# Performance work log

Hardware: AMD Instinct MI355X
Metric: run time of the kernel (lower is better)

Reference implementation:

```python
import jax, jax.numpy as jnp
import numpy as np

N_HEADS = 16


def setup_inputs() -> dict:
    key = jax.random.key(0)
    k1, k2, k3 = jax.random.split(key, 3)
    B, T, C = 4, 2048, 1024
    x = jax.random.normal(k1, (B, T, C), dtype=jnp.float32)
    # nn.Linear weights: init ~ U(-1/sqrt(fan_in), 1/sqrt(fan_in)); scaled normal is fine for a reference
    w_qkv = jax.random.normal(k2, (C, 3 * C), dtype=jnp.float32) * (1.0 / np.sqrt(C))
    w_out = jax.random.normal(k3, (C, C), dtype=jnp.float32) * (1.0 / np.sqrt(C))
    return {"x": x, "w_qkv": w_qkv, "w_out": w_out}


def reference(x, w_qkv, w_out):
    B, T, C = x.shape
    H = N_HEADS
    D = C // H  # head_dim
    qkv = x @ w_qkv  # [B, T, 3C]
    q, k, v = jnp.split(qkv, 3, axis=-1)
    # [B, H, T, D]
    q = q.reshape(B, T, H, D).transpose(0, 2, 1, 3)
    k = k.reshape(B, T, H, D).transpose(0, 2, 1, 3)
    v = v.reshape(B, T, H, D).transpose(0, 2, 1, 3)
    scale = 1.0 / np.sqrt(D)
    scores = jnp.einsum('bhqd,bhkd->bhqk', q, k) * scale  # [B, H, T, T]
    causal = jnp.tril(jnp.ones((T, T), dtype=bool))
    scores = jnp.where(causal[None, None, :, :], scores, -jnp.inf)
    weights = jax.nn.softmax(scores, axis=-1)
    out = jnp.einsum('bhqk,bhkd->bhqd', weights, v)  # [B, H, T, D]
    out = out.transpose(0, 2, 1, 3).reshape(B, T, C)
    return out @ w_out
```

## Files before the change

kernel.cpp:

```cpp
#include <hip/hip_runtime.h>
#include <hip/hip_bf16.h>
#include <math.h>
#include <type_traits>

using s16x8 = __attribute__((ext_vector_type(8))) short;
using s16x4 = __attribute__((ext_vector_type(4))) short;
using f32x4 = __attribute__((ext_vector_type(4))) float;
using f32x16 = __attribute__((ext_vector_type(16))) float;
using u32 = unsigned int;
using u32x4 = __attribute__((ext_vector_type(4))) u32;

static __device__ __forceinline__ short f2bf(float f) {
  union { float f; unsigned u; } v; v.f = f;
  unsigned r = v.u + 0x7fff + ((v.u >> 16) & 1);
  return (short)(r >> 16);
}

static __device__ __forceinline__ unsigned cvt_pk_bf16(float lo, float hi) {
  unsigned r;
  asm("v_cvt_pk_bf16_f32 %0, %1, %2" : "=v"(r) : "v"(lo), "v"(hi));
  return r;
}

#define GLOAD_LDS(gsrc, ldst)                                                      \
  __builtin_amdgcn_global_load_lds(                                                \
      (const __attribute__((address_space(1))) void*)(gsrc),                       \
      (__attribute__((address_space(3))) void*)(ldst), 16, 0, 0)

__global__ void cast_f32_bf16(const float* __restrict__ in, short* __restrict__ out, int n4) {
  int i = blockIdx.x * blockDim.x + threadIdx.x;
  int stride = gridDim.x * blockDim.x;
  for (int idx = i; idx < n4; idx += stride) {
    float4 v = reinterpret_cast<const float4*>(in)[idx];
    s16x4 o; o[0] = f2bf(v.x); o[1] = f2bf(v.y); o[2] = f2bf(v.z); o[3] = f2bf(v.w);
    reinterpret_cast<s16x4*>(out)[idx] = o;
  }
}

__global__ void transpose_cast(const float* __restrict__ in, short* __restrict__ out, int R, int C) {
  __shared__ float tile[32][33];
  int cb = blockIdx.x * 32, rb = blockIdx.y * 32;
  int tx = threadIdx.x, ty = threadIdx.y;
  #pragma unroll
  for (int i = 0; i < 32; i += 8)
    tile[ty + i][tx] = in[(size_t)(rb + ty + i) * C + cb + tx];
  __syncthreads();
  #pragma unroll
  for (int i = 0; i < 32; i += 8)
    out[(size_t)(cb + ty + i) * R + rb + tx] = f2bf(tile[tx][ty + i]);
}

template <typename OutT, bool VFUSE>
__global__ __launch_bounds__(256) void gemm_bt(const short* __restrict__ A,
                                               const short* __restrict__ BT,
                                               OutT* __restrict__ C,
                                               short* __restrict__ vtOut,
                                               int M, int N, int K, int ldc) {
  __shared__ __align__(16) short As[128][32];
  __shared__ __align__(16) short Bs[128][32];
  const int t = threadIdx.x;
  const int lane = t & 63, wid = t >> 6;
  const int wm = wid >> 1, wn = wid & 1;
  const int bm = blockIdx.y * 128, bn = blockIdx.x * 128;
  const int lr = lane & 15, lg = lane >> 4;

  f32x4 acc[4][4] = {};

  for (int k0 = 0; k0 < K; k0 += 32) {
    #pragma unroll
    for (int rnd = 0; rnd < 2; ++rnd) {
      int chunk = rnd * 256 + t;
      int row = chunk >> 2, c8 = (chunk & 3) * 8;
      GLOAD_LDS(&A[(size_t)(bm + row) * K + k0 + c8], &As[rnd * 64 + wid * 16][0]);
      GLOAD_LDS(&BT[(size_t)(bn + row) * K + k0 + c8], &Bs[rnd * 64 + wid * 16][0]);
    }
    __syncthreads();
    s16x8 af[4], bfr[4];
    #pragma unroll
    for (int i = 0; i < 4; ++i)
      af[i] = *reinterpret_cast<s16x8*>(&As[wm * 64 + i * 16 + lr][lg * 8]);
    #pragma unroll
    for (int j = 0; j < 4; ++j)
      bfr[j] = *reinterpret_cast<s16x8*>(&Bs[wn * 64 + j * 16 + lr][lg * 8]);
    #pragma unroll
    for (int i = 0; i < 4; ++i)
      #pragma unroll
      for (int j = 0; j < 4; ++j)
        acc[i][j] = __builtin_amdgcn_mfma_f32_16x16x32_bf16(af[i], bfr[j], acc[i][j], 0, 0, 0);
    __syncthreads();
  }

  const int r0 = bm + wm * 64, c0 = bn + wn * 64;
  if (!VFUSE || c0 < 2048) {
    #pragma unroll
    for (int i = 0; i < 4; ++i)
      #pragma unroll
      for (int j = 0; j < 4; ++j)
        #pragma unroll
        for (int r = 0; r < 4; ++r) {
          int row = r0 + i * 16 + lg * 4 + r;
          int col = c0 + j * 16 + lr;
          float v = acc[i][j][r];
          if constexpr (std::is_same<OutT, short>::value)
            C[(size_t)row * ldc + col] = f2bf(v);
          else
            C[(size_t)row * ldc + col] = v;
        }
  } else {
    const int bb = bm >> 11;
    #pragma unroll
    for (int i = 0; i < 4; ++i) {
      int tok = (bm & 2047) + wm * 64 + i * 16 + lg * 4;
      #pragma unroll
      for (int j = 0; j < 4; ++j) {
        int col = c0 + j * 16 + lr;
        s16x4 p;
        #pragma unroll
        for (int r = 0; r < 4; ++r) p[r] = f2bf(acc[i][j][r]);
        *reinterpret_cast<s16x4*>(vtOut + (size_t)(bb * 1024 + col - 2048) * 2048 + tok) = p;
      }
    }
  }
}

__global__ __launch_bounds__(256, 3) void attn_kernel(const short* __restrict__ qk,
                                                      const short* __restrict__ vt,
                                                      short* __restrict__ att) {
  const int T = 2048, C2 = 2048, Cc = 1024;
  const int fid = blockIdx.x;
  const int qb = 15 - (fid >> 6);
  const int bh = fid & 63;
  const int h = bh & 15, b = bh >> 4;
  const int t = threadIdx.x;
  const int w = t >> 6, l = t & 63;
  const int q2 = l & 31, hi = l >> 5;

  __shared__ __align__(16) short Ks[2][64 * 64];
  __shared__ __align__(16) short Vts[2][64 * 64];

  const int qrow_base = qb * 128 + w * 32;
  const int qrow = qrow_base + q2;
  const int tmax = 2 * qb + (w >> 1);
  const int nt = 2 * qb + 2;

  const float SC = 0.125f * 1.44269504088896340736f;
  s16x8 aq[4];
  #pragma unroll
  for (int ds = 0; ds < 4; ++ds) {
    s16x8 q = *reinterpret_cast<const s16x8*>(
        qk + (size_t)(b * T + qrow) * C2 + h * 64 + ds * 16 + hi * 8);
    #pragma unroll
    for (int j = 0; j < 8; ++j) {
      union { float f; unsigned u; } v; v.u = ((unsigned)(unsigned short)q[j]) << 16;
      q[j] = f2bf(v.f * SC);
    }
    aq[ds] = q;
  }

  f32x16 o[2] = {};
  float mst = -INFINITY, lst = 0.f;

  const int srow = w * 16 + (l >> 3);
  const int srcc8 = ((l & 7) ^ (l >> 3)) * 8;
  const short* kp = qk + (size_t)(b * T + srow) * C2 + Cc + h * 64 + srcc8;
  const short* vp = vt + (size_t)(bh * 64 + srow) * T + srcc8;

  auto stage = [&](int buf) {
    GLOAD_LDS(kp,           &Ks[buf][(w * 16) * 64]);
    GLOAD_LDS(kp + 8 * C2,  &Ks[buf][(w * 16 + 8) * 64]);
    GLOAD_LDS(vp,           &Vts[buf][(w * 16) * 64]);
    GLOAD_LDS(vp + 8 * T,   &Vts[buf][(w * 16 + 8) * 64]);
    kp += 64 * C2;
    vp += 64;
  };

  stage(0);
  for (int tt = 0; tt < nt; ++tt) {
    __syncthreads();
    if (tt + 1 < nt) stage((tt + 1) & 1);
    if (tt > tmax) continue;
    const int j0 = tt << 6;
    const short* K_ = &Ks[tt & 1][0];
    const short* V_ = &Vts[tt & 1][0];

    f32x16 st[2];
    __builtin_amdgcn_s_setprio(1);
    #pragma unroll
    for (int kt = 0; kt < 2; ++kt) {
      f32x16 s = {};
      #pragma unroll
      for (int ds = 0; ds < 4; ++ds) {
        int row = kt * 32 + q2;
        s16x8 ak = *reinterpret_cast<const s16x8*>(
            &K_[row * 64 + (((ds * 2 + hi) ^ (row & 7)) * 8)]);
        s = __builtin_amdgcn_mfma_f32_32x32x16_bf16(ak, aq[ds], s, 0, 0, 0);
      }
      st[kt] = s;
    }
    __builtin_amdgcn_s_setprio(0);

    if (j0 + 63 > qrow_base) {
      #pragma unroll
      for (int kt = 0; kt < 2; ++kt)
        #pragma unroll
        for (int r = 0; r < 16; ++r) {
          int key = j0 + kt * 32 + (r & 3) + 8 * (r >> 2) + 4 * hi;
          if (key > qrow) st[kt][r] = -INFINITY;
        }
    }

    float a16[16];
    #pragma unroll
    for (int r = 0; r < 16; ++r) a16[r] = fmaxf(st[0][r], st[1][r]);
    #pragma unroll
    for (int r = 0; r < 8; ++r) a16[r] = fmaxf(a16[r], a16[r + 8]);
    #pragma unroll
    for (int r = 0; r < 4; ++r) a16[r] = fmaxf(a16[r], a16[r + 4]);
    float mx = fmaxf(fmaxf(a16[0], a16[1]), fmaxf(a16[2], a16[3]));
    mx = fmaxf(mx, __shfl_xor(mx, 32));
    const bool resc = !__all(mx - mst <= 8.f);
    if (resc) {
      float mn = fmaxf(mst, mx);
      float corr = exp2f(mst - mn);
      mst = mn;
      lst *= corr;
      #pragma unroll
      for (int dt = 0; dt < 2; ++dt)
        #pragma unroll
        for (int r = 0; r < 16; ++r) o[dt][r] *= corr;
    }
    #pragma unroll
    for (int kt = 0; kt < 2; ++kt)
      #pragma unroll
      for (int r = 0; r < 16; ++r) st[kt][r] = exp2f(st[kt][r] - mst);
    float sv[16];
    #pragma unroll
    for (int r = 0; r < 16; ++r) sv[r] = st[0][r] + st[1][r];
    #pragma unroll
    for (int r = 0; r < 8; ++r) sv[r] += sv[r + 8];
    #pragma unroll
    for (int r = 0; r < 4; ++r) sv[r] += sv[r + 4];
    float ps = (sv[0] + sv[1]) + (sv[2] + sv[3]);
    ps += __shfl_xor(ps, 32);
    lst += ps;

    s16x8 pb[4];
    #pragma unroll
    for (int kt = 0; kt < 2; ++kt)
      #pragma unroll
      for (int s = 0; s < 2; ++s) {
        unsigned w01 = cvt_pk_bf16(st[kt][s * 8 + 0], st[kt][s * 8 + 1]);
        unsigned w23 = cvt_pk_bf16(st[kt][s * 8 + 2], st[kt][s * 8 + 3]);
        unsigned w45 = cvt_pk_bf16(st[kt][s * 8 + 4], st[kt][s * 8 + 5]);
        unsigned w67 = cvt_pk_bf16(st[kt][s * 8 + 6], st[kt][s * 8 + 7]);
        asm("v_permlane32_swap_b32 %0, %1" : "+v"(w01), "+v"(w45));
        asm("v_permlane32_swap_b32 %0, %1" : "+v"(w23), "+v"(w67));
        u32x4 f; f[0] = w01; f[1] = w23; f[2] = w45; f[3] = w67;
        pb[kt * 2 + s] = *reinterpret_cast<s16x8*>(&f);
      }

    __builtin_amdgcn_s_setprio(1);
    #pragma unroll
    for (int dt = 0; dt < 2; ++dt) {
      int row = dt * 32 + q2;
      #pragma unroll
      for (int ks = 0; ks < 4; ++ks) {
        s16x8 av = *reinterpret_cast<const s16x8*>(
            &V_[row * 64 + (((ks * 2 + hi) ^ (row & 7)) * 8)]);
        o[dt] = __builtin_amdgcn_mfma_f32_32x32x16_bf16(av, pb[ks], o[dt], 0, 0, 0);
      }
    }
    __builtin_amdgcn_s_setprio(0);
  }

  __syncthreads();
  u32* osm = reinterpret_cast<u32*>(&Ks[0][0]) + w * 1024;
  float inv = 1.f / lst;
  #pragma unroll
  for (int dt = 0; dt < 2; ++dt)
    #pragma unroll
    for (int p = 0; p < 8; ++p) {
      unsigned pk = ((unsigned)(unsigned short)f2bf(o[dt][2 * p + 1] * inv) << 16)
                  | (unsigned)(unsigned short)f2bf(o[dt][2 * p] * inv);
      int col = dt * 16 + (p >> 1) * 4 + 2 * hi + (p & 1);
      int chunk = col >> 2, inc = col & 3;
      osm[q2 * 32 + ((chunk ^ (q2 & 7)) * 4) + inc] = pk;
    }
  #pragma unroll
  for (int c = 0; c < 4; ++c) {
    int chunk = hi * 4 + c;
    u32x4 v4 = *reinterpret_cast<u32x4*>(&osm[q2 * 32 + ((chunk ^ (q2 & 7)) * 4)]);
    *reinterpret_cast<u32x4*>(
        att + (size_t)(b * T + qrow_base + q2) * Cc + h * 64 + chunk * 8) = v4;
  }
}

extern "C" void kernel_launch(void* const* d_in, const int* in_sizes, int n_in,
                              void* d_out, int out_size, void* d_ws, size_t ws_size,
                              hipStream_t stream) {
  const float* x     = (const float*)d_in[0];
  const float* w_qkv = (const float*)d_in[1];
  const float* w_out = (const float*)d_in[2];
  float* out = (float*)d_out;

  char* ws = (char*)d_ws;
  short* xb    = (short*)(ws);
  short* wqkvT = (short*)(ws + 16777216);
  short* woT   = (short*)(ws + 23068672);
  short* qk    = (short*)(ws + 25165824);
  short* vtb   = (short*)(ws + 58720256);
  short* att   = (short*)(ws + 75497472);

  cast_f32_bf16<<<2048, 256, 0, stream>>>(x, xb, (8192 * 1024) / 4);
  transpose_cast<<<dim3(3072 / 32, 1024 / 32), dim3(32, 8), 0, stream>>>(w_qkv, wqkvT, 1024, 3072);
  transpose_cast<<<dim3(1024 / 32, 1024 / 32), dim3(32, 8), 0, stream>>>(w_out, woT, 1024, 1024);

  gemm_bt<short, true><<<dim3(3072 / 128, 8192 / 128), 256, 0, stream>>>(
      xb, wqkvT, qk, vtb, 8192, 3072, 1024, 2048);
  attn_kernel<<<1024, 256, 0, stream>>>(qk, vtb, att);
  gemm_bt<float, false><<<dim3(1024 / 128, 8192 / 128), 256, 0, stream>>>(
      att, woT, out, nullptr, 8192, 1024, 1024, 1024);
}
```

Before: 194.9 us.

## Double-buffer GEMM LDS tiles with BK=64, XOR swizzle, and block remap

Restructures the bf16 GEMM main loop to use two LDS buffers with a K-tile of 64, so the global-to-LDS load of the next tile overlaps the MFMA work on the current one and one barrier per iteration is removed. LDS rows are XOR-swizzled by row index to avoid bank conflicts on the fragment reads. Workgroup IDs are remapped in groups of 8, which is meant to improve L2 locality or spread tiles across XCDs. LDS usage grows fourfold, which may reduce occupancy.

```diff
diff --git a/kernel.cpp b/kernel.cpp
--- a/kernel.cpp
+++ b/kernel.cpp
@@ -56,38 +56,62 @@
                                                OutT* __restrict__ C,
                                                short* __restrict__ vtOut,
                                                int M, int N, int K, int ldc) {
-  __shared__ __align__(16) short As[128][32];
-  __shared__ __align__(16) short Bs[128][32];
+  __shared__ __align__(16) short As[2][128 * 64];
+  __shared__ __align__(16) short Bs[2][128 * 64];
   const int t = threadIdx.x;
   const int lane = t & 63, wid = t >> 6;
   const int wm = wid >> 1, wn = wid & 1;
-  const int bm = blockIdx.y * 128, bn = blockIdx.x * 128;
   const int lr = lane & 15, lg = lane >> 4;
 
+  const int gx = gridDim.x;
+  const int nwg = gx * gridDim.y;
+  int fid = blockIdx.y * gx + blockIdx.x;
+  fid = (fid & 7) * (nwg >> 3) + (fid >> 3);
+  const int bn = (fid % gx) * 128;
+  const int bm = (fid / gx) * 128;
+
+  const int srow = lane >> 3;
+  const int schunk = (lane & 7) ^ srow;
+  const short* ap = A + (size_t)(bm + wid * 8 + srow) * K + schunk * 8;
+  const short* bp = BT + (size_t)(bn + wid * 8 + srow) * K + schunk * 8;
+
   f32x4 acc[4][4] = {};
-
-  for (int k0 = 0; k0 < K; k0 += 32) {
-    #pragma unroll
-    for (int rnd = 0; rnd < 2; ++rnd) {
-      int chunk = rnd * 256 + t;
-      int row = chunk >> 2, c8 = (chunk & 3) * 8;
-      GLOAD_LDS(&A[(size_t)(bm + row) * K + k0 + c8], &As[rnd * 64 + wid * 16][0]);
-      GLOAD_LDS(&BT[(size_t)(bn + row) * K + k0 + c8], &Bs[rnd * 64 + wid * 16][0]);
-    }
+  const int nk = K >> 6;
+
+  auto stage = [&](int buf, int kt) {
+    const size_t ko = (size_t)kt << 6;
+    #pragma unroll
+    for (int j = 0; j < 4; ++j) {
+      GLOAD_LDS(ap + (size_t)j * 32 * K + ko, &As[buf][(j * 32 + wid * 8) * 64]);
+      GLOAD_LDS(bp + (size_t)j * 32 * K + ko, &Bs[buf][(j * 32 + wid * 8) * 64]);
+    }
+  };
+
+  stage(0, 0);
+  for (int kt = 0; kt < nk; ++kt) {
     __syncthreads();
-    s16x8 af[4], bfr[4];
-    #pragma unroll
-    for (int i = 0; i < 4; ++i)
-      af[i] = *reinterpret_cast<s16x8*>(&As[wm * 64 + i * 16 + lr][lg * 8]);
-    #pragma unroll
-    for (int j = 0; j < 4; ++j)
-      bfr[j] = *reinterpret_cast<s16x8*>(&Bs[wn * 64 + j * 16 + lr][lg * 8]);
-    #pragma unroll
-    for (int i = 0; i < 4; ++i)
-      #pragma unroll
-      for (int j = 0; j < 4; ++j)
-        acc[i][j] = __builtin_amdgcn_mfma_f32_16x16x32_bf16(af[i], bfr[j], acc[i][j], 0, 0, 0);
-    __syncthreads();
+    if (kt + 1 < nk) stage((kt + 1) & 1, kt + 1);
+    const short* A_ = &As[kt & 1][0];
+    const short* B_ = &Bs[kt & 1][0];
+    #pragma unroll
+    for (int ks = 0; ks < 2; ++ks) {
+      s16x8 af[4], bfr[4];
+      #pragma unroll
+      for (int i = 0; i < 4; ++i) {
+        int r = wm * 64 + i * 16 + lr;
+        af[i] = *reinterpret_cast<const s16x8*>(&A_[r * 64 + (((ks * 4 + lg) ^ (r & 7)) * 8)]);
+      }
+      #pragma unroll
+      for (int j = 0; j < 4; ++j) {
+        int r = wn * 64 + j * 16 + lr;
+        bfr[j] = *reinterpret_cast<const s16x8*>(&B_[r * 64 + (((ks * 4 + lg) ^ (r & 7)) * 8)]);
+      }
+      #pragma unroll
+      for (int i = 0; i < 4; ++i)
+        #pragma unroll
+        for (int j = 0; j < 4; ++j)
+          acc[i][j] = __builtin_amdgcn_mfma_f32_16x16x32_bf16(af[i], bfr[j], acc[i][j], 0, 0, 0);
+    }
   }
 
   const int r0 = bm + wm * 64, c0 = bn + wn * 64;
```

New measurement: 174.5 us. 10.5% less time.
